# Optimization experiments

Hardware: AMD Instinct MI355X
Metric: run time of the kernel (lower is better)

Reference implementation:

```python
import jax, jax.numpy as jnp
from jax import lax
import numpy as np

WIN_SIZE = 11
WIN_SIGMA = 1.5
DATA_RANGE = 1.0
K1, K2 = 0.01, 0.03
DN = ('NCHW', 'OIHW', 'NCHW')


def _gauss_1d(size, sigma):
    coords = jnp.arange(size, dtype=jnp.float32) - (size // 2)
    g = jnp.exp(-coords ** 2 / (2.0 * sigma ** 2))
    return g / g.sum()


def _gaussian_filter(x, g):
    # depthwise separable valid conv: along W then along H (order irrelevant)
    C = x.shape[1]
    kw = jnp.tile(g.reshape(1, 1, 1, -1), (C, 1, 1, 1))  # [C,1,1,K]
    kh = jnp.tile(g.reshape(1, 1, -1, 1), (C, 1, 1, 1))  # [C,1,K,1]
    x = lax.conv_general_dilated(x, kw, (1, 1), 'VALID',
                                 feature_group_count=C, dimension_numbers=DN)
    x = lax.conv_general_dilated(x, kh, (1, 1), 'VALID',
                                 feature_group_count=C, dimension_numbers=DN)
    return x


def setup_inputs() -> dict:
    key = jax.random.key(0)
    k1, k2 = jax.random.split(key)
    X = jax.random.uniform(k1, (32, 3, 512, 512), dtype=jnp.float32, minval=-1.0, maxval=1.0)
    Y = jax.random.uniform(k2, (32, 3, 512, 512), dtype=jnp.float32, minval=-1.0, maxval=1.0)
    return {"X": X, "Y": Y}


def reference(X, Y):
    # channel == 3 -> normalize from [-1,1] to [0,1]
    X = (X + 1.0) / 2.0
    Y = (Y + 1.0) / 2.0

    g = _gauss_1d(WIN_SIZE, WIN_SIGMA).astype(X.dtype)
    C1 = (K1 * DATA_RANGE) ** 2
    C2 = (K2 * DATA_RANGE) ** 2

    mu1 = _gaussian_filter(X, g)
    mu2 = _gaussian_filter(Y, g)
    mu1_sq = mu1 * mu1
    mu2_sq = mu2 * mu2
    mu1_mu2 = mu1 * mu2

    sigma1_sq = _gaussian_filter(X * X, g) - mu1_sq
    sigma2_sq = _gaussian_filter(Y * Y, g) - mu2_sq
    sigma12 = _gaussian_filter(X * Y, g) - mu1_mu2

    cs_map = (2.0 * sigma12 + C2) / (sigma1_sq + sigma2_sq + C2)
    ssim_map = (2.0 * mu1_mu2 + C1) / (mu1_sq + mu2_sq + C1) * cs_map

    # size_average=True, full=False -> scalar mean SSIM
    return ssim_map.mean()
```

## Files before the change

### kernel.cpp

```cpp
#include <hip/hip_runtime.h>
#include <cmath>


#define HH 512
#define WW 512
#define OH 502
#define OW 502
#define NC 96
#define TXS 32
#define TYB 64
#define INR 74
#define HP4 33
#define GX 16
#define GY 8
#define NTASK (INR * 8)
#define NSLOT 64

typedef float f4 __attribute__((ext_vector_type(4)));

struct GaussW { float g[11]; };

static __device__ __forceinline__ f4 sp(float s) { return (f4){s, s, s, s}; }

__global__ __launch_bounds__(256, 4) void ssim_kernel(
        const float* __restrict__ X, const float* __restrict__ Y,
        double* __restrict__ acc, GaussW gw) {
    __shared__ f4 hS[INR][HP4];
    __shared__ double wsum[4];

    const int tid = threadIdx.x;
    const int R0 = blockIdx.y * TYB;
    const int C0 = blockIdx.x * TXS;
    const float* Xp = X + (size_t)blockIdx.z * (HH * WW);
    const float* Yp = Y + (size_t)blockIdx.z * (HH * WW);
    const bool edge = (blockIdx.x == GX - 1);

    for (int t = tid; t < NTASK; t += 256) {
        int r, cg;
        if (t < 576) { r = (t & 7) | ((t >> 6) << 3); cg = (t >> 3) & 7; }
        else         { int tt = t - 576; r = 72 + (tt & 1); cg = (tt >> 1) & 7; }
        const int gr = min(R0 + r, HH - 1);
        const float* xrow = Xp + gr * WW;
        const float* yrow = Yp + gr * WW;
        const int gc = C0 + 4 * cg;

        float xv[16], yv[16];
        if (!edge) {
            const float4* x4 = (const float4*)(xrow + gc);
            const float4* y4 = (const float4*)(yrow + gc);
            float4 a0 = x4[0], a1 = x4[1], a2 = x4[2], a3 = x4[3];
            float4 b0 = y4[0], b1 = y4[1], b2 = y4[2], b3 = y4[3];
            xv[0]=a0.x; xv[1]=a0.y; xv[2]=a0.z; xv[3]=a0.w;
            xv[4]=a1.x; xv[5]=a1.y; xv[6]=a1.z; xv[7]=a1.w;
            xv[8]=a2.x; xv[9]=a2.y; xv[10]=a2.z; xv[11]=a2.w;
            xv[12]=a3.x; xv[13]=a3.y; xv[14]=a3.z; xv[15]=a3.w;
            yv[0]=b0.x; yv[1]=b0.y; yv[2]=b0.z; yv[3]=b0.w;
            yv[4]=b1.x; yv[5]=b1.y; yv[6]=b1.z; yv[7]=b1.w;
            yv[8]=b2.x; yv[9]=b2.y; yv[10]=b2.z; yv[11]=b2.w;
            yv[12]=b3.x; yv[13]=b3.y; yv[14]=b3.z; yv[15]=b3.w;
        } else {
            #pragma unroll
            for (int i = 0; i < 16; ++i) {
                int c = min(gc + i, WW - 1);
                xv[i] = xrow[c];
                yv[i] = yrow[c];
            }
        }

        f4 a0v = sp(0.f), a1v = sp(0.f), a2v = sp(0.f), a3v = sp(0.f);
        #pragma unroll
        for (int k = 0; k < 14; ++k) {
            float x = xv[k], y = yv[k];
            f4 P;
            P.x = x; P.y = y;
            P.z = fmaf(x, x, y * y);
            P.w = x * y;
            #pragma unroll
            for (int j = 0; j < 4; ++j) {
                int u = k - j;
                if (u >= 0 && u < 11) {
                    f4 G = sp(gw.g[u]);
                    if (j == 0) a0v = __builtin_elementwise_fma(G, P, a0v);
                    if (j == 1) a1v = __builtin_elementwise_fma(G, P, a1v);
                    if (j == 2) a2v = __builtin_elementwise_fma(G, P, a2v);
                    if (j == 3) a3v = __builtin_elementwise_fma(G, P, a3v);
                }
            }
        }
        hS[r][4 * cg + 0] = a0v;
        hS[r][4 * cg + 1] = a1v;
        hS[r][4 * cg + 2] = a2v;
        hS[r][4 * cg + 3] = a3v;
    }
    __syncthreads();

    const int c  = tid & 31;
    const int rb = (tid >> 5) * 8;
    f4 A[8];
    #pragma unroll
    for (int j = 0; j < 8; ++j) A[j] = sp(0.f);
    #pragma unroll
    for (int k = 0; k < 18; ++k) {
        f4 v = hS[rb + k][c];
        #pragma unroll
        for (int j = 0; j < 8; ++j) {
            int u = k - j;
            if (u >= 0 && u < 11) {
                f4 G = sp(gw.g[u]);
                A[j] = __builtin_elementwise_fma(G, v, A[j]);
            }
        }
    }

    const float C1 = 1.0e-4f;
    const float C2 = 9.0e-4f;
    float nn[8], dd[8];
    #pragma unroll
    for (int j = 0; j < 8; ++j) {
        f4 v = A[j];
        float t1 = v.x + 1.f, t2 = v.y + 1.f;
        float num1 = fmaf(t1 * t2, 0.5f, C1);
        float den1 = fmaf(fmaf(t2, t2, t1 * t1), 0.25f, C1);
        float num2 = fmaf(v.w - v.x * v.y, 0.5f, C2);
        float den2 = fmaf(v.z - fmaf(v.x, v.x, v.y * v.y), 0.25f, C2);
        bool valid = (R0 + rb + j < OH) & (C0 + c < OW);
        nn[j] = valid ? num1 * num2 : 0.f;
        dd[j] = valid ? den1 * den2 : 1.f;
    }
    double tsum = 0.0;
    #pragma unroll
    for (int g = 0; g < 8; g += 4) {
        float d01 = dd[g] * dd[g + 1], d23 = dd[g + 2] * dd[g + 3];
        float s01 = fmaf(nn[g], dd[g + 1], nn[g + 1] * dd[g]);
        float s23 = fmaf(nn[g + 2], dd[g + 3], nn[g + 3] * dd[g + 2]);
        tsum += (double)(fmaf(s01, d23, s23 * d01) / (d01 * d23));
    }

    #pragma unroll
    for (int off = 32; off > 0; off >>= 1)
        tsum += __shfl_down(tsum, off, 64);
    if ((tid & 63) == 0) wsum[tid >> 6] = tsum;
    __syncthreads();
    if (tid == 0) {
        int slot = (blockIdx.x + blockIdx.y * GX + blockIdx.z * GX * GY) & (NSLOT - 1);
        atomicAdd(&acc[slot * 8], wsum[0] + wsum[1] + wsum[2] + wsum[3]);
    }
}

__global__ void ssim_finalize(const double* __restrict__ acc,
                              float* __restrict__ out) {
    int lane = threadIdx.x;
    double t = acc[lane * 8];
    #pragma unroll
    for (int off = 32; off > 0; off >>= 1)
        t += __shfl_down(t, off, 64);
    if (lane == 0)
        out[0] = (float)(t * (1.0 / (double)((long long)NC * OH * OW)));
}

extern "C" void kernel_launch(void* const* d_in, const int* in_sizes, int n_in,
                              void* d_out, int out_size, void* d_ws, size_t ws_size,
                              hipStream_t stream) {
    const float* X = (const float*)d_in[0];
    const float* Y = (const float*)d_in[1];
    float* out = (float*)d_out;
    double* acc = (double*)d_ws;

    hipMemsetAsync(d_ws, 0, NSLOT * 64, stream);

    GaussW gw;
    {
        double g[11], s = 0.0;
        for (int i = 0; i < 11; ++i) {
            double d = (double)(i - 5);
            g[i] = exp(-d * d / (2.0 * 1.5 * 1.5));
            s += g[i];
        }
        for (int i = 0; i < 11; ++i) gw.g[i] = (float)(g[i] / s);
    }

    dim3 grid(GX, GY, NC);
    ssim_kernel<<<grid, dim3(256), 0, stream>>>(X, Y, acc, gw);
    ssim_finalize<<<1, dim3(64), 0, stream>>>(acc, out);
}
```

Before: 294.8 us.

## Retile rows to 54 per block and issue all input loads up front with inline asm

Changes the row tile from 64 to 54 output rows (GY 8->10), so each block needs exactly 64 input rows, which gives two tasks per thread with no tail loop. All sixteen dwordx4 global loads per thread are issued together through inline asm, with partial s_waitcnt so the first task's horizontal convolution overlaps the second task's loads. Each vertical thread now computes 7 output rows, and padded LDS rows are zeroed with the extra rows masked out. This trades some redundant halo reads and extra blocks for better memory-level parallelism, and relies on fragile inline-asm waitcnt ordering.

```diff
diff --git a/kernel.cpp b/kernel.cpp
--- a/kernel.cpp
+++ b/kernel.cpp
@@ -8,12 +8,12 @@
 #define OW 502
 #define NC 96
 #define TXS 32
-#define TYB 64
-#define INR 74
+#define TYB 54
+#define INRD 64
+#define INRS 66
 #define HP4 33
 #define GX 16
-#define GY 8
-#define NTASK (INR * 8)
+#define GY 10
 #define NSLOT 64
 
 typedef float f4 __attribute__((ext_vector_type(4)));
@@ -21,11 +21,15 @@
 struct GaussW { float g[11]; };
 
 static __device__ __forceinline__ f4 sp(float s) { return (f4){s, s, s, s}; }
+
+#define GLD(dst, p, o) \
+    asm volatile("global_load_dwordx4 %0, %1, off offset:" #o \
+                 : "=v"(dst) : "v"(p) : "memory")
 
 __global__ __launch_bounds__(256, 4) void ssim_kernel(
         const float* __restrict__ X, const float* __restrict__ Y,
         double* __restrict__ acc, GaussW gw) {
-    __shared__ f4 hS[INR][HP4];
+    __shared__ f4 hS[INRS][HP4];
     __shared__ double wsum[4];
 
     const int tid = threadIdx.x;
@@ -35,38 +39,19 @@
     const float* Yp = Y + (size_t)blockIdx.z * (HH * WW);
     const bool edge = (blockIdx.x == GX - 1);
 
-    for (int t = tid; t < NTASK; t += 256) {
-        int r, cg;
-        if (t < 576) { r = (t & 7) | ((t >> 6) << 3); cg = (t >> 3) & 7; }
-        else         { int tt = t - 576; r = 72 + (tt & 1); cg = (tt >> 1) & 7; }
-        const int gr = min(R0 + r, HH - 1);
-        const float* xrow = Xp + gr * WW;
-        const float* yrow = Yp + gr * WW;
-        const int gc = C0 + 4 * cg;
-
+    if (tid < 2 * HP4) {
+        int rr = tid / HP4;
+        hS[INRD + rr][tid - rr * HP4] = sp(0.f);
+    }
+
+    auto hconv = [&](int r, int cg, f4 X0, f4 X1, f4 X2, f4 X3,
+                     f4 Y0, f4 Y1, f4 Y2, f4 Y3) {
         float xv[16], yv[16];
-        if (!edge) {
-            const float4* x4 = (const float4*)(xrow + gc);
-            const float4* y4 = (const float4*)(yrow + gc);
-            float4 a0 = x4[0], a1 = x4[1], a2 = x4[2], a3 = x4[3];
-            float4 b0 = y4[0], b1 = y4[1], b2 = y4[2], b3 = y4[3];
-            xv[0]=a0.x; xv[1]=a0.y; xv[2]=a0.z; xv[3]=a0.w;
-            xv[4]=a1.x; xv[5]=a1.y; xv[6]=a1.z; xv[7]=a1.w;
-            xv[8]=a2.x; xv[9]=a2.y; xv[10]=a2.z; xv[11]=a2.w;
-            xv[12]=a3.x; xv[13]=a3.y; xv[14]=a3.z; xv[15]=a3.w;
-            yv[0]=b0.x; yv[1]=b0.y; yv[2]=b0.z; yv[3]=b0.w;
-            yv[4]=b1.x; yv[5]=b1.y; yv[6]=b1.z; yv[7]=b1.w;
-            yv[8]=b2.x; yv[9]=b2.y; yv[10]=b2.z; yv[11]=b2.w;
-            yv[12]=b3.x; yv[13]=b3.y; yv[14]=b3.z; yv[15]=b3.w;
-        } else {
-            #pragma unroll
-            for (int i = 0; i < 16; ++i) {
-                int c = min(gc + i, WW - 1);
-                xv[i] = xrow[c];
-                yv[i] = yrow[c];
-            }
-        }
-
+        #pragma unroll
+        for (int i = 0; i < 4; ++i) {
+            xv[i] = X0[i]; xv[4 + i] = X1[i]; xv[8 + i] = X2[i]; xv[12 + i] = X3[i];
+            yv[i] = Y0[i]; yv[4 + i] = Y1[i]; yv[8 + i] = Y2[i]; yv[12 + i] = Y3[i];
+        }
         f4 a0v = sp(0.f), a1v = sp(0.f), a2v = sp(0.f), a3v = sp(0.f);
         #pragma unroll
         for (int k = 0; k < 14; ++k) {
@@ -91,19 +76,66 @@
         hS[r][4 * cg + 1] = a1v;
         hS[r][4 * cg + 2] = a2v;
         hS[r][4 * cg + 3] = a3v;
+    };
+
+    auto taskEdge = [&](int r, int cg) {
+        const int gr = min(R0 + r, HH - 1);
+        const float* xrow = Xp + gr * WW;
+        const float* yrow = Yp + gr * WW;
+        const int gc = C0 + 4 * cg;
+        f4 xv4[4], yv4[4];
+        #pragma unroll
+        for (int i = 0; i < 16; ++i) {
+            int c = min(gc + i, WW - 1);
+            xv4[i >> 2][i & 3] = xrow[c];
+            yv4[i >> 2][i & 3] = yrow[c];
+        }
+        hconv(r, cg, xv4[0], xv4[1], xv4[2], xv4[3],
+                     yv4[0], yv4[1], yv4[2], yv4[3]);
+    };
+
+    {
+        const int r0 = (tid & 7) | ((tid >> 6) << 3);
+        const int g0 = (tid >> 3) & 7;
+        const int t1 = tid + 256;
+        const int r1 = (t1 & 7) | ((t1 >> 6) << 3);
+        const int g1 = (t1 >> 3) & 7;
+        if (!edge) {
+            const float* px0 = Xp + min(R0 + r0, HH - 1) * WW + C0 + 4 * g0;
+            const float* py0 = Yp + min(R0 + r0, HH - 1) * WW + C0 + 4 * g0;
+            const float* px1 = Xp + min(R0 + r1, HH - 1) * WW + C0 + 4 * g1;
+            const float* py1 = Yp + min(R0 + r1, HH - 1) * WW + C0 + 4 * g1;
+            f4 xa0, xa1, xa2, xa3, ya0, ya1, ya2, ya3;
+            f4 xb0, xb1, xb2, xb3, yb0, yb1, yb2, yb3;
+            GLD(xa0, px0, 0); GLD(xa1, px0, 16); GLD(xa2, px0, 32); GLD(xa3, px0, 48);
+            GLD(ya0, py0, 0); GLD(ya1, py0, 16); GLD(ya2, py0, 32); GLD(ya3, py0, 48);
+            GLD(xb0, px1, 0); GLD(xb1, px1, 16); GLD(xb2, px1, 32); GLD(xb3, px1, 48);
+            GLD(yb0, py1, 0); GLD(yb1, py1, 16); GLD(yb2, py1, 32); GLD(yb3, py1, 48);
+            asm volatile("s_waitcnt vmcnt(8)"
+                : "+v"(xa0), "+v"(xa1), "+v"(xa2), "+v"(xa3),
+                  "+v"(ya0), "+v"(ya1), "+v"(ya2), "+v"(ya3) :: "memory");
+            hconv(r0, g0, xa0, xa1, xa2, xa3, ya0, ya1, ya2, ya3);
+            asm volatile("s_waitcnt vmcnt(0)"
+                : "+v"(xb0), "+v"(xb1), "+v"(xb2), "+v"(xb3),
+                  "+v"(yb0), "+v"(yb1), "+v"(yb2), "+v"(yb3) :: "memory");
+            hconv(r1, g1, xb0, xb1, xb2, xb3, yb0, yb1, yb2, yb3);
+        } else {
+            taskEdge(r0, g0);
+            taskEdge(r1, g1);
+        }
     }
     __syncthreads();
 
     const int c  = tid & 31;
-    const int rb = (tid >> 5) * 8;
-    f4 A[8];
-    #pragma unroll
-    for (int j = 0; j < 8; ++j) A[j] = sp(0.f);
-    #pragma unroll
-    for (int k = 0; k < 18; ++k) {
+    const int rb = 7 * (tid >> 5);
+    f4 A[7];
+    #pragma unroll
+    for (int j = 0; j < 7; ++j) A[j] = sp(0.f);
+    #pragma unroll
+    for (int k = 0; k < 17; ++k) {
         f4 v = hS[rb + k][c];
         #pragma unroll
-        for (int j = 0; j < 8; ++j) {
+        for (int j = 0; j < 7; ++j) {
             int u = k - j;
             if (u >= 0 && u < 11) {
                 f4 G = sp(gw.g[u]);
@@ -114,26 +146,29 @@
 
     const float C1 = 1.0e-4f;
     const float C2 = 9.0e-4f;
-    float nn[8], dd[8];
-    #pragma unroll
-    for (int j = 0; j < 8; ++j) {
+    float nn[7], dd[7];
+    #pragma unroll
+    for (int j = 0; j < 7; ++j) {
         f4 v = A[j];
         float t1 = v.x + 1.f, t2 = v.y + 1.f;
         float num1 = fmaf(t1 * t2, 0.5f, C1);
         float den1 = fmaf(fmaf(t2, t2, t1 * t1), 0.25f, C1);
         float num2 = fmaf(v.w - v.x * v.y, 0.5f, C2);
         float den2 = fmaf(v.z - fmaf(v.x, v.x, v.y * v.y), 0.25f, C2);
-        bool valid = (R0 + rb + j < OH) & (C0 + c < OW);
+        bool valid = (rb + j < TYB) & (R0 + rb + j < OH) & (C0 + c < OW);
         nn[j] = valid ? num1 * num2 : 0.f;
         dd[j] = valid ? den1 * den2 : 1.f;
     }
     double tsum = 0.0;
-    #pragma unroll
-    for (int g = 0; g < 8; g += 4) {
-        float d01 = dd[g] * dd[g + 1], d23 = dd[g + 2] * dd[g + 3];
-        float s01 = fmaf(nn[g], dd[g + 1], nn[g + 1] * dd[g]);
-        float s23 = fmaf(nn[g + 2], dd[g + 3], nn[g + 3] * dd[g + 2]);
+    {
+        float d01 = dd[0] * dd[1], d23 = dd[2] * dd[3];
+        float s01 = fmaf(nn[0], dd[1], nn[1] * dd[0]);
+        float s23 = fmaf(nn[2], dd[3], nn[3] * dd[2]);
         tsum += (double)(fmaf(s01, d23, s23 * d01) / (d01 * d23));
+        float d45 = dd[4] * dd[5];
+        float s45 = fmaf(nn[4], dd[5], nn[5] * dd[4]);
+        float num = fmaf(s45, dd[6], nn[6] * d45);
+        tsum += (double)(num / (d45 * dd[6]));
     }
 
     #pragma unroll
```

New measurement: 330.2 us. 12.0% more time.

## Stage raw tiles into LDS via async global_load_lds and shrink row tiles

Applied to the files above, without the earlier changes.

Input rows of X and Y are now copied straight into shared memory with global_load_lds. The horizontal Gaussian pass then reads from LDS instead of issuing per-thread global vector loads, and the separate right-edge path goes away. The tile height drops from 64 to 30 output rows, so the grid has more blocks and each thread's vertical pass computes 4 outputs instead of 8. The aim is better latency hiding and occupancy, paid for with a larger halo fraction (redundant rows and horizontal work) and more LDS per block.

```diff
diff --git a/kernel.cpp b/kernel.cpp
--- a/kernel.cpp
+++ b/kernel.cpp
@@ -8,12 +8,14 @@
 #define OW 502
 #define NC 96
 #define TXS 32
-#define TYB 64
-#define INR 74
+#define TYB 30
+#define INR 40
+#define INRS 42
+#define RAWP 13
+#define NRAW (INR*RAWP)
 #define HP4 33
 #define GX 16
-#define GY 8
-#define NTASK (INR * 8)
+#define GY 17
 #define NSLOT 64
 
 typedef float f4 __attribute__((ext_vector_type(4)));
@@ -25,7 +27,8 @@
 __global__ __launch_bounds__(256, 4) void ssim_kernel(
         const float* __restrict__ X, const float* __restrict__ Y,
         double* __restrict__ acc, GaussW gw) {
-    __shared__ f4 hS[INR][HP4];
+    __shared__ f4 rawS[2 * NRAW];
+    __shared__ f4 hS[INRS][HP4];
     __shared__ double wsum[4];
 
     const int tid = threadIdx.x;
@@ -33,40 +36,38 @@
     const int C0 = blockIdx.x * TXS;
     const float* Xp = X + (size_t)blockIdx.z * (HH * WW);
     const float* Yp = Y + (size_t)blockIdx.z * (HH * WW);
-    const bool edge = (blockIdx.x == GX - 1);
 
-    for (int t = tid; t < NTASK; t += 256) {
-        int r, cg;
-        if (t < 576) { r = (t & 7) | ((t >> 6) << 3); cg = (t >> 3) & 7; }
-        else         { int tt = t - 576; r = 72 + (tt & 1); cg = (tt >> 1) & 7; }
-        const int gr = min(R0 + r, HH - 1);
-        const float* xrow = Xp + gr * WW;
-        const float* yrow = Yp + gr * WW;
-        const int gc = C0 + 4 * cg;
+    #pragma unroll
+    for (int k = 0; k < 5; ++k) {
+        int i = (k << 8) + tid;
+        if (i < 2 * NRAW) {
+            int a  = i >= NRAW;
+            int j  = a ? i - NRAW : i;
+            int r  = j / RAWP;
+            int c4 = j - r * RAWP;
+            const float* bp  = a ? Yp : Xp;
+            const float* src = bp + min(R0 + r, HH - 1) * WW
+                                  + min(C0 + 4 * c4, WW - 4);
+            f4* dst = &rawS[i & ~63];
+            __builtin_amdgcn_global_load_lds(
+                (const __attribute__((address_space(1))) void*)src,
+                (__attribute__((address_space(3))) void*)dst, 16, 0, 0);
+        }
+    }
+    __syncthreads();
 
+    auto task = [&](int r, int cg) {
+        const int ib = RAWP * r + cg;
+        f4 x0 = rawS[ib + 0], x1 = rawS[ib + 1];
+        f4 x2 = rawS[ib + 2], x3 = rawS[ib + 3];
+        f4 y0 = rawS[NRAW + ib + 0], y1 = rawS[NRAW + ib + 1];
+        f4 y2 = rawS[NRAW + ib + 2], y3 = rawS[NRAW + ib + 3];
         float xv[16], yv[16];
-        if (!edge) {
-            const float4* x4 = (const float4*)(xrow + gc);
-            const float4* y4 = (const float4*)(yrow + gc);
-            float4 a0 = x4[0], a1 = x4[1], a2 = x4[2], a3 = x4[3];
-            float4 b0 = y4[0], b1 = y4[1], b2 = y4[2], b3 = y4[3];
-            xv[0]=a0.x; xv[1]=a0.y; xv[2]=a0.z; xv[3]=a0.w;
-            xv[4]=a1.x; xv[5]=a1.y; xv[6]=a1.z; xv[7]=a1.w;
-            xv[8]=a2.x; xv[9]=a2.y; xv[10]=a2.z; xv[11]=a2.w;
-            xv[12]=a3.x; xv[13]=a3.y; xv[14]=a3.z; xv[15]=a3.w;
-            yv[0]=b0.x; yv[1]=b0.y; yv[2]=b0.z; yv[3]=b0.w;
-            yv[4]=b1.x; yv[5]=b1.y; yv[6]=b1.z; yv[7]=b1.w;
-            yv[8]=b2.x; yv[9]=b2.y; yv[10]=b2.z; yv[11]=b2.w;
-            yv[12]=b3.x; yv[13]=b3.y; yv[14]=b3.z; yv[15]=b3.w;
-        } else {
-            #pragma unroll
-            for (int i = 0; i < 16; ++i) {
-                int c = min(gc + i, WW - 1);
-                xv[i] = xrow[c];
-                yv[i] = yrow[c];
-            }
+        #pragma unroll
+        for (int i = 0; i < 4; ++i) {
+            xv[i] = x0[i]; xv[4 + i] = x1[i]; xv[8 + i] = x2[i]; xv[12 + i] = x3[i];
+            yv[i] = y0[i]; yv[4 + i] = y1[i]; yv[8 + i] = y2[i]; yv[12 + i] = y3[i];
         }
-
         f4 a0v = sp(0.f), a1v = sp(0.f), a2v = sp(0.f), a3v = sp(0.f);
         #pragma unroll
         for (int k = 0; k < 14; ++k) {
@@ -91,19 +92,24 @@
         hS[r][4 * cg + 1] = a1v;
         hS[r][4 * cg + 2] = a2v;
         hS[r][4 * cg + 3] = a3v;
+    };
+    {
+        const int cg = (tid >> 3) & 7;
+        task((tid & 7) | ((tid >> 6) << 3), cg);
+        if (tid < 64) task((tid & 7) | 32, cg);
     }
     __syncthreads();
 
     const int c  = tid & 31;
-    const int rb = (tid >> 5) * 8;
-    f4 A[8];
+    const int rb = (tid >> 5) * 4;
+    f4 A[4];
     #pragma unroll
-    for (int j = 0; j < 8; ++j) A[j] = sp(0.f);
+    for (int j = 0; j < 4; ++j) A[j] = sp(0.f);
     #pragma unroll
-    for (int k = 0; k < 18; ++k) {
+    for (int k = 0; k < 14; ++k) {
         f4 v = hS[rb + k][c];
         #pragma unroll
-        for (int j = 0; j < 8; ++j) {
+        for (int j = 0; j < 4; ++j) {
             int u = k - j;
             if (u >= 0 && u < 11) {
                 f4 G = sp(gw.g[u]);
@@ -114,27 +120,23 @@
 
     const float C1 = 1.0e-4f;
     const float C2 = 9.0e-4f;
-    float nn[8], dd[8];
+    float nn[4], dd[4];
     #pragma unroll
-    for (int j = 0; j < 8; ++j) {
+    for (int j = 0; j < 4; ++j) {
         f4 v = A[j];
         float t1 = v.x + 1.f, t2 = v.y + 1.f;
         float num1 = fmaf(t1 * t2, 0.5f, C1);
         float den1 = fmaf(fmaf(t2, t2, t1 * t1), 0.25f, C1);
         float num2 = fmaf(v.w - v.x * v.y, 0.5f, C2);
         float den2 = fmaf(v.z - fmaf(v.x, v.x, v.y * v.y), 0.25f, C2);
-        bool valid = (R0 + rb + j < OH) & (C0 + c < OW);
+        bool valid = (rb + j < TYB) & (R0 + rb + j < OH) & (C0 + c < OW);
         nn[j] = valid ? num1 * num2 : 0.f;
         dd[j] = valid ? den1 * den2 : 1.f;
     }
-    double tsum = 0.0;
-    #pragma unroll
-    for (int g = 0; g < 8; g += 4) {
-        float d01 = dd[g] * dd[g + 1], d23 = dd[g + 2] * dd[g + 3];
-        float s01 = fmaf(nn[g], dd[g + 1], nn[g + 1] * dd[g]);
-        float s23 = fmaf(nn[g + 2], dd[g + 3], nn[g + 3] * dd[g + 2]);
-        tsum += (double)(fmaf(s01, d23, s23 * d01) / (d01 * d23));
-    }
+    float d01 = dd[0] * dd[1], d23 = dd[2] * dd[3];
+    float s01 = fmaf(nn[0], dd[1], nn[1] * dd[0]);
+    float s23 = fmaf(nn[2], dd[3], nn[3] * dd[2]);
+    double tsum = (double)(fmaf(s01, d23, s23 * d01) / (d01 * d23));
 
     #pragma unroll
     for (int off = 32; off > 0; off >>= 1)
```

Result: faster. 261.7 us (-11.2%).
